# Kernel tuning notes

Hardware: AMD Instinct MI355X
Metric: run time of the kernel (lower is better)

Reference implementation:

```python
import jax, jax.numpy as jnp
import numpy as np

NUM_C, BS, L, D, M = 4096, 32, 512, 128, 50
TA, TB, TC = 0.075, 0.088, 1.0  # triangular membership params


def setup_inputs() -> dict:
    key = jax.random.key(0)
    ks = jax.random.split(key, 16)
    g = lambda i, shape, s: jax.random.normal(ks[i], shape, jnp.float32) * s
    return {
        "q": jax.random.randint(ks[0], (BS, L), 0, NUM_C),
        "r": jax.random.randint(ks[1], (BS, L), 0, 2),
        "k_emb": g(2, (NUM_C, D), 1.0),
        "Mk": g(3, (M, D), (2.0 / D) ** 0.5),
        "Mv0": g(4, (M, D), (2.0 / D) ** 0.5),
        "f_W": g(5, (D, 2 * D), (1.0 / (2 * D)) ** 0.5),
        "f_b": jnp.zeros((D,), jnp.float32),
        "a_W": g(6, (D, NUM_C + D), (1.0 / (NUM_C + D)) ** 0.5),
        "a_b": jnp.zeros((D,), jnp.float32),
        "e_W": g(7, (D, D), (2.0 / D) ** 0.5),
        "e_b": jnp.zeros((D,), jnp.float32),
        "add_W": g(8, (D, D), (2.0 / D) ** 0.5),
        "add_b": jnp.zeros((D,), jnp.float32),
        "Wih": g(9, (4 * D, D), (1.0 / D) ** 0.5),
        "Whh": g(10, (4 * D, D), (1.0 / D) ** 0.5),
        "bih": jnp.zeros((4 * D,), jnp.float32),
        "bhh": jnp.zeros((4 * D,), jnp.float32),
        "p_W": g(11, (1, D), (1.0 / D) ** 0.5),
        "p_b": jnp.zeros((1,), jnp.float32),
    }


def _forward(q, r, k_emb, Mk, Mv0, f_W, f_b, a_W, a_b, e_W, e_b,
             add_W, add_b, Wih, Whh, bih, bhh, p_W, p_b):
    B, T = q.shape
    k = k_emb[q]                                    # (B,L,D) key embeddings
    # a_embed = Linear(num_c + dim_s, dim_s) on concat(one_hot(q)*r, f):
    # split the weight so the one-hot matmul becomes a gather.
    a_Wq, a_Wf = a_W[:, :NUM_C], a_W[:, NUM_C:]
    yq = a_Wq.T[q] * r[..., None].astype(k.dtype)   # (B,L,D)

    def mem_step(Mv, xs):
        k_t, yq_t = xs                              # (B,D), (B,D)
        w = jax.nn.softmax(k_t @ Mk.T, axis=1)      # (B,M) addressing
        read = jnp.einsum('bm,bmd->bd', w, Mv)      # weighted read
        f = jnp.tanh(jnp.concatenate([read, k_t], 1) @ f_W.T + f_b)
        y = yq_t + f @ a_Wf.T + a_b                 # write content
        e = jax.nn.sigmoid(y @ e_W.T + e_b)         # erase gate
        a = jnp.tanh(y @ add_W.T + add_b)           # add vector
        Mv = Mv * (1.0 - w[:, :, None] * e[:, None, :]) + w[:, :, None] * a[:, None, :]
        return Mv, (w, f)

    Mv0b = jnp.broadcast_to(Mv0, (B, M, D))
    _, (w_all, f_all) = jax.lax.scan(
        mem_step, Mv0b, (k.transpose(1, 0, 2), yq.transpose(1, 0, 2)))
    w_all = w_all.transpose(1, 0, 2)                # (B,L,M)
    f_all = f_all.transpose(1, 0, 2)                # (B,L,D)

    # triangular membership -> ternary identity vectors {0,1,2}
    tw = jnp.maximum(jnp.minimum((w_all - TA) / (TB - TA),
                                 (TC - w_all) / (TC - TB)), 0.0)
    iv = jnp.where(tw >= 0.6, 2.0, jnp.where(tw >= 0.1, 1.0, 0.0))
    sq = jnp.sum(iv * iv, axis=2)                   # (B,L)
    dist = sq[:, :, None] + sq[:, None, :] - 2.0 * jnp.einsum('bim,bjm->bij', iv, iv)
    NEG = jnp.float32(-1e32)
    dist = jnp.where(dist > 0.0, NEG, dist)
    ut = jnp.triu(jnp.ones((T, T), bool), k=0)      # mask j >= i
    dist = jnp.where(ut[None], NEG, dist)
    idx = jnp.arange(T * T, dtype=dist.dtype).reshape(T, T)
    final = dist + idx[None]                        # (B,L,L)
    matched = jnp.max(final, axis=2) >= 0.0         # (B,L) has identical prev step
    prev = jnp.argmax(final, axis=2)                # (B,L) most recent identical t'

    # hop-LSTM: reuse hidden/cell state of previous identical timestep
    barange = jnp.arange(B)
    h0 = jnp.zeros((B, D), k.dtype)
    H0 = jnp.zeros((T, B, D), k.dtype)

    def lstm_step(carry, xs):
        h, c, H, C = carry
        t, f_t, m_t, p_t = xs
        h_in = jnp.where(m_t[:, None], H[p_t, barange], h)
        c_in = jnp.where(m_t[:, None], C[p_t, barange], c)
        gates = f_t @ Wih.T + bih + h_in @ Whh.T + bhh
        i_g, f_g, g_g, o_g = jnp.split(gates, 4, axis=1)  # torch order i,f,g,o
        c_new = jax.nn.sigmoid(f_g) * c_in + jax.nn.sigmoid(i_g) * jnp.tanh(g_g)
        h_new = jax.nn.sigmoid(o_g) * jnp.tanh(c_new)
        return (h_new, c_new, H.at[t].set(h_new), C.at[t].set(c_new)), h_new

    _, h_all = jax.lax.scan(
        lstm_step, (h0, h0, H0, H0),
        (jnp.arange(T), f_all.transpose(1, 0, 2), matched.T, prev.T))
    h_all = h_all.transpose(1, 0, 2)                # (B,L,D)
    # dropout is identity in eval mode
    p = jax.nn.sigmoid(h_all @ p_W.T + p_b)[..., 0]  # (B,L)
    return p


def reference(q, r, k_emb, Mk, Mv0, f_W, f_b, a_W, a_b, e_W, e_b,
              add_W, add_b, Wih, Whh, bih, bhh, p_W, p_b):
    return _forward(q, r, k_emb, Mk, Mv0, f_W, f_b, a_W, a_b, e_W, e_b,
                    add_W, add_b, Wih, Whh, bih, bhh, p_W, p_b)
```

## Files before the change

### kernel.cpp

```cpp
#include <hip/hip_runtime.h>
#include <cstdint>
#include <cstddef>

#define NUM_C 4096
#define BB 32
#define TT 512
#define DD 128
#define MM 50

using ull = unsigned long long;

__device__ __forceinline__ float sigmoidf_(float x){ return 1.0f/(1.0f + expf(-x)); }

__device__ __forceinline__ float fexp2_(float x){ return __builtin_amdgcn_exp2f(x); }
__device__ __forceinline__ float frcp_(float x){ return __builtin_amdgcn_rcpf(x); }
__device__ __forceinline__ float fast_sig_(float x){
  return frcp_(1.0f + fexp2_(-1.44269504088896341f*x));
}
__device__ __forceinline__ float fast_tanh_(float x){
  float t = fexp2_(2.88539008177792681f*x);
  return 1.0f - 2.0f*frcp_(t + 1.0f);
}

__device__ __forceinline__ float quadSum_(float v){
  int t = __builtin_amdgcn_update_dpp(0, __float_as_int(v), 0xB1, 0xF, 0xF, true);
  v += __int_as_float(t);
  t = __builtin_amdgcn_update_dpp(0, __float_as_int(v), 0x4E, 0xF, 0xF, true);
  v += __int_as_float(t);
  return v;
}

__device__ __forceinline__ void barL_(){
  asm volatile("s_waitcnt lgkmcnt(0)\n\ts_barrier" ::: "memory");
}
__device__ __forceinline__ void waitVM_(){
  asm volatile("s_waitcnt vmcnt(0)" ::: "memory");
}

__global__ __launch_bounds__(256) void kPre(
    const int* __restrict__ q, const int* __restrict__ r,
    const float* __restrict__ k_emb, const float* __restrict__ Mk,
    const float* __restrict__ f_W, const float* __restrict__ f_b,
    const float* __restrict__ a_W, const float* __restrict__ a_b,
    float* __restrict__ wAll, ull* __restrict__ keyLo, ull* __restrict__ keyHi,
    float* __restrict__ fpre, float* __restrict__ ypre)
{
  const int b = blockIdx.y, t0 = blockIdx.x * 32, tid = threadIdx.x;
  __shared__ __align__(16) float sK[32*129];
  __shared__ int sQ[32];
  __shared__ int sR[32];
  __shared__ union UU {
    struct { float sMk[MM*129]; double sZ[32*MM]; } p2;
    float sW2[128*65];
  } u;

  if (tid < 32){ sQ[tid] = q[b*TT + t0 + tid]; sR[tid] = r[b*TT + t0 + tid]; }
  __syncthreads();
  for (int i = tid; i < 32*128; i += 256){
    int tl = i >> 7, j = i & 127;
    sK[tl*129 + j] = k_emb[(size_t)sQ[tl]*DD + j];
  }
  for (int i = tid; i < MM*128; i += 256){
    int m = i >> 7, j = i & 127;
    u.p2.sMk[m*129 + j] = Mk[i];
  }
  __syncthreads();

  for (int idx = tid; idx < 32*MM; idx += 256){
    int tl = idx / MM, m = idx - tl*MM;
    double z = 0.0;
    for (int j = 0; j < DD; j++)
      z += (double)sK[tl*129 + j] * (double)u.p2.sMk[m*129 + j];
    u.p2.sZ[tl*MM + m] = z;
  }
  __syncthreads();

  {
    int tl = tid >> 3, l8 = tid & 7;
    double zmax = -1e300;
    for (int m = l8; m < MM; m += 8) zmax = fmax(zmax, u.p2.sZ[tl*MM + m]);
    for (int s = 1; s < 8; s <<= 1) zmax = fmax(zmax, __shfl_xor(zmax, s));
    double se = 0.0;
    for (int m = l8; m < MM; m += 8){
      double e = exp(u.p2.sZ[tl*MM + m] - zmax);
      u.p2.sZ[tl*MM + m] = e;
      se += e;
    }
    for (int s = 1; s < 8; s <<= 1) se += __shfl_xor(se, s);
    double inv = 1.0 / se;
    ull klo = 0, khi = 0;
    for (int m = l8; m < MM; m += 8){
      double w = u.p2.sZ[tl*MM + m] * inv;
      wAll[((size_t)(b*TT + t0 + tl))*MM + m] = (float)w;
      double tw = fmin((w - 0.075)/(0.088 - 0.075), (1.0 - w)/(1.0 - 0.088));
      tw = fmax(tw, 0.0);
      ull iv = (tw >= 0.6) ? 2ull : ((tw >= 0.1) ? 1ull : 0ull);
      if (m < 32) klo |= iv << (2*m); else khi |= iv << (2*(m-32));
    }
    for (int s = 1; s < 8; s <<= 1){ klo |= __shfl_xor(klo, s); khi |= __shfl_xor(khi, s); }
    if (l8 == 0){ keyLo[b*TT + t0 + tl] = klo; keyHi[b*TT + t0 + tl] = khi; }
  }

  {
    const int dq = tid & 31, tq = tid >> 5;
    float acc[4][4];
    #pragma unroll
    for (int a = 0; a < 4; a++){ acc[a][0]=0.f; acc[a][1]=0.f; acc[a][2]=0.f; acc[a][3]=0.f; }
    for (int jh = 0; jh < 2; jh++){
      __syncthreads();
      for (int i = tid; i < 128*64; i += 256){
        int dd = i >> 6, jj = i & 63;
        u.sW2[dd*65 + jj] = f_W[dd*256 + 128 + jh*64 + jj];
      }
      __syncthreads();
      for (int jj = 0; jj < 64; jj++){
        float kv[4], wv[4];
        #pragma unroll
        for (int a = 0; a < 4; a++) kv[a] = sK[(tq*4 + a)*129 + jh*64 + jj];
        #pragma unroll
        for (int c = 0; c < 4; c++) wv[c] = u.sW2[(dq*4 + c)*65 + jj];
        #pragma unroll
        for (int a = 0; a < 4; a++){
          acc[a][0] += kv[a]*wv[0]; acc[a][1] += kv[a]*wv[1];
          acc[a][2] += kv[a]*wv[2]; acc[a][3] += kv[a]*wv[3];
        }
      }
    }
    #pragma unroll
    for (int a = 0; a < 4; a++){
      int tl = tq*4 + a;
      #pragma unroll
      for (int c = 0; c < 4; c++){
        int d = dq*4 + c;
        fpre[((size_t)(b*TT + t0 + tl))*DD + d] = acc[a][c] + f_b[d];
      }
    }
  }

  for (int i = tid; i < 32*DD; i += 256){
    int tl = i >> 7, d = i & 127;
    ypre[((size_t)(b*TT + t0 + tl))*DD + d] =
        a_W[(size_t)d*(NUM_C + DD) + sQ[tl]] * (float)sR[tl] + a_b[d];
  }
}

__global__ __launch_bounds__(512) void kMatch(
    const ull* __restrict__ keyLo, const ull* __restrict__ keyHi, int* __restrict__ prevA)
{
  const int b = blockIdx.x, i = threadIdx.x;
  __shared__ ull slo[TT];
  __shared__ ull shi[TT];
  slo[i] = keyLo[b*TT + i];
  shi[i] = keyHi[b*TT + i];
  __syncthreads();
  const ull mylo = slo[i], myhi = shi[i];
  int found = -1;
  for (int j = i - 1; j >= 0; j--){
    if (slo[j] == mylo && shi[j] == myhi){ found = j; break; }
  }
  prevA[b*TT + i] = found;
}

__global__ __launch_bounds__(128) void kWW(
    const float* __restrict__ e_W, const float* __restrict__ add_W,
    const float* __restrict__ a_W,
    float* __restrict__ Ge, float* __restrict__ Ga)
{
  const int d = blockIdx.x;
  const int k = threadIdx.x;
  __shared__ float se[128];
  __shared__ float sa[128];
  se[k] = e_W[(size_t)d*DD + k];
  sa[k] = add_W[(size_t)d*DD + k];
  __syncthreads();
  float ge = 0.f, ga = 0.f;
  for (int j = 0; j < DD; j++){
    float af = a_W[(size_t)j*(NUM_C + DD) + NUM_C + k];
    ge += se[j]*af;
    ga += sa[j]*af;
  }
  Ge[(size_t)d*DD + k] = ge;
  Ga[(size_t)d*DD + k] = ga;
}

__global__ __launch_bounds__(256) void kEA(
    const float* __restrict__ ypre, const float* __restrict__ e_W,
    const float* __restrict__ add_W, const float* __restrict__ e_b,
    const float* __restrict__ add_b, float* __restrict__ eapre)
{
  const int jt = blockIdx.x;
  const int rt = blockIdx.y;
  const int tid = threadIdx.x;
  __shared__ float sW[64*129];
  __shared__ float sF[32*129];
  for (int i = tid; i < 64*128; i += 256){
    int jj = i >> 7, k = i & 127;
    int j = jt*64 + jj;
    sW[jj*129 + k] = (j < 128) ? e_W[(size_t)j*DD + k] : add_W[(size_t)(j-128)*DD + k];
  }
  for (int i = tid; i < 32*128; i += 256){
    int rr = i >> 7, k = i & 127;
    sF[rr*129 + k] = ypre[(size_t)(rt*32 + rr)*DD + k];
  }
  __syncthreads();
  const int jq = tid & 31, rq = tid >> 5;
  float acc[4][2];
  #pragma unroll
  for (int a = 0; a < 4; a++){ acc[a][0] = 0.f; acc[a][1] = 0.f; }
  for (int k = 0; k < 128; k++){
    float fv[4], wv[2];
    #pragma unroll
    for (int a = 0; a < 4; a++) fv[a] = sF[(rq*4 + a)*129 + k];
    wv[0] = sW[(jq*2 + 0)*129 + k];
    wv[1] = sW[(jq*2 + 1)*129 + k];
    #pragma unroll
    for (int a = 0; a < 4; a++){ acc[a][0] += fv[a]*wv[0]; acc[a][1] += fv[a]*wv[1]; }
  }
  #pragma unroll
  for (int a = 0; a < 4; a++){
    int rowi = rt*32 + rq*4 + a;
    #pragma unroll
    for (int c = 0; c < 2; c++){
      int j = jt*64 + jq*2 + c;
      float bj = (j < 128) ? e_b[j] : add_b[j - 128];
      eapre[(size_t)rowi*256 + j] = acc[a][c] + bj;
    }
  }
}

__global__ __launch_bounds__(256) void kWih4(
    const float* __restrict__ Wih, float* __restrict__ Wih4)
{
  int idx = blockIdx.x*256 + threadIdx.x;
  int j = idx >> 7, k = idx & 127;
  Wih4[(size_t)(k >> 2)*2048 + j*4 + (k & 3)] = Wih[idx];
}

__global__ __launch_bounds__(512, 2) __attribute__((amdgpu_waves_per_eu(2, 2)))
void kFused(
    const float* __restrict__ wAll, const float* __restrict__ fpre,
    const float* __restrict__ eapre, const float* __restrict__ f_W,
    const float* __restrict__ Ge, const float* __restrict__ Ga,
    const float* __restrict__ Mv0, float* __restrict__ fAll,
    const float* __restrict__ Wih4, const float* __restrict__ bih,
    const float* __restrict__ bhh, const int* __restrict__ prevA,
    const float* __restrict__ Whh, float* __restrict__ Hh,
    float* __restrict__ Ch, float* __restrict__ gpre, int* __restrict__ prog)
{
  const int tid = threadIdx.x;
  const int b = blockIdx.x & 31;
  const size_t base = (size_t)b*TT;

  __shared__ __align__(16) union SU {
    struct {
      float bufR[144]; float bufF[144]; float sW9[9*52];
      float sF8[8*128]; float sEA8[8*256]; float fO8[8*128];
    } m;
    struct { float sFc[8*128]; } g;
    struct {
      float xh[2][144]; float gbuf[8*512]; int spv[TT];
      float hRing[8*128]; float cRing[8*128];
    } l;
  } su;

  if (blockIdx.x < 32){
    const int dd = tid >> 2, kc = tid & 3, m0 = kc*13;
    const int wslot = (dd >> 5)*36 + (dd & 31);

    float mv[13];
    #pragma unroll
    for (int i = 0; i < 13; i++){
      int m = m0 + i;
      mv[i] = (m < MM) ? Mv0[(size_t)m*DD + dd] : 0.f;
    }
    float wf[32], ge[32], ga[32];
    {
      const float4* p;
      p = reinterpret_cast<const float4*>(&f_W[dd*256 + kc*32]);
      #pragma unroll
      for (int i = 0; i < 8; i++){ float4 v = p[i]; wf[4*i]=v.x; wf[4*i+1]=v.y; wf[4*i+2]=v.z; wf[4*i+3]=v.w; }
      p = reinterpret_cast<const float4*>(&Ge[(size_t)dd*DD + kc*32]);
      #pragma unroll
      for (int i = 0; i < 8; i++){ float4 v = p[i]; ge[4*i]=v.x; ge[4*i+1]=v.y; ge[4*i+2]=v.z; ge[4*i+3]=v.w; }
      p = reinterpret_cast<const float4*>(&Ga[(size_t)dd*DD + kc*32]);
      #pragma unroll
      for (int i = 0; i < 8; i++){ float4 v = p[i]; ga[4*i]=v.x; ga[4*i+1]=v.y; ga[4*i+2]=v.z; ga[4*i+3]=v.w; }
    }

    const int rr0 = tid / 50, mm0 = tid - rr0*50;
    if (tid < 18){ int rr = tid >> 1; su.m.sW9[rr*52 + 50 + (tid & 1)] = 0.f; }

    float4 pF = {0.f,0.f,0.f,0.f}, pEA = {0.f,0.f,0.f,0.f};
    float pW = 0.f;
    if (tid < 256) pF = reinterpret_cast<const float4*>(&fpre[base*DD])[tid];
    pEA = reinterpret_cast<const float4*>(&eapre[base*256])[tid];
    if (tid < 450) pW = wAll[(base + rr0)*MM + mm0];

    float wreg[13];

    for (int ch = 0; ch < TT/8; ch++){
      const int t0 = ch*8;
      if (ch){
        if (tid < 256){
          float4 v = reinterpret_cast<const float4*>(su.m.fO8)[tid];
          float* dst = &fAll[(base + t0 - 8)*DD + tid*4];
          __hip_atomic_store(dst+0, v.x, __ATOMIC_RELAXED, __HIP_MEMORY_SCOPE_AGENT);
          __hip_atomic_store(dst+1, v.y, __ATOMIC_RELAXED, __HIP_MEMORY_SCOPE_AGENT);
          __hip_atomic_store(dst+2, v.z, __ATOMIC_RELAXED, __HIP_MEMORY_SCOPE_AGENT);
          __hip_atomic_store(dst+3, v.w, __ATOMIC_RELAXED, __HIP_MEMORY_SCOPE_AGENT);
        }
      }
      if (tid < 256) reinterpret_cast<float4*>(su.m.sF8)[tid] = pF;
      reinterpret_cast<float4*>(su.m.sEA8)[tid] = pEA;
      if (tid < 450) su.m.sW9[rr0*52 + mm0] = pW;
      if (ch && tid < 256) waitVM_();
      if (t0 + 8 < TT){
        if (tid < 256) pF = reinterpret_cast<const float4*>(&fpre[(base + t0 + 8)*DD])[tid];
        pEA = reinterpret_cast<const float4*>(&eapre[(base + t0 + 8)*256])[tid];
        if (tid < 450) pW = (t0 + 8 + rr0 < TT) ? wAll[(base + t0 + 8 + rr0)*MM + mm0] : 0.f;
      }
      barL_();
      if (ch && tid == 0)
        __hip_atomic_store(&prog[b], ch, __ATOMIC_RELAXED, __HIP_MEMORY_SCOPE_AGENT);

      if (ch == 0){
        #pragma unroll
        for (int i = 0; i < 13; i++) wreg[i] = su.m.sW9[m0 + i];
        float r = 0.f;
        #pragma unroll
        for (int i = 0; i < 13; i++) r += wreg[i]*mv[i];
        r = quadSum_(r);
        if (kc == 0) su.m.bufR[wslot] = r;
        barL_();
      }

      #pragma unroll
      for (int tc = 0; tc < 8; tc++){
        float wn[13];
        #pragma unroll
        for (int i = 0; i < 13; i++) wn[i] = su.m.sW9[(tc+1)*52 + m0 + i];

        {
          const float4* x4 = reinterpret_cast<const float4*>(&su.m.bufR[kc*36]);
          float a0=0.f,a1=0.f,a2=0.f,a3=0.f;
          #pragma unroll
          for (int i = 0; i < 8; i++){
            float4 xv = x4[i];
            a0 += xv.x*wf[4*i]; a1 += xv.y*wf[4*i+1]; a2 += xv.z*wf[4*i+2]; a3 += xv.w*wf[4*i+3];
          }
          float s = quadSum_((a0+a1)+(a2+a3));
          float fval = fast_tanh_(s + su.m.sF8[tc*128 + dd]);
          if (kc == 0){
            su.m.bufF[wslot] = fval;
            su.m.fO8[tc*128 + dd] = fval;
          }
        }
        barL_();

        {
          const float4* x4 = reinterpret_cast<const float4*>(&su.m.bufF[kc*36]);
          float e0=0.f,e1=0.f,g0=0.f,g1=0.f;
          #pragma unroll
          for (int i = 0; i < 8; i++){
            float4 xv = x4[i];
            e0 += xv.x*ge[4*i];   e1 += xv.y*ge[4*i+1];
            e0 += xv.z*ge[4*i+2]; e1 += xv.w*ge[4*i+3];
            g0 += xv.x*ga[4*i];   g1 += xv.y*ga[4*i+1];
            g0 += xv.z*ga[4*i+2]; g1 += xv.w*ga[4*i+3];
          }
          float ep = quadSum_(e0 + e1);
          float ap = quadSum_(g0 + g1);
          float e_d = fast_sig_(ep + su.m.sEA8[tc*256 + dd]);
          float a_d = fast_tanh_(ap + su.m.sEA8[tc*256 + 128 + dd]);
          float rp0 = 0.f, rp1 = 0.f;
          #pragma unroll
          for (int i = 0; i < 13; i++){
            float t = __builtin_fmaf(-e_d, mv[i], a_d);
            mv[i] = __builtin_fmaf(wreg[i], t, mv[i]);
            if (i & 1) rp1 = __builtin_fmaf(wn[i], mv[i], rp1);
            else       rp0 = __builtin_fmaf(wn[i], mv[i], rp0);
          }
          float rd = quadSum_(rp0 + rp1);
          if (kc == 0) su.m.bufR[wslot] = rd;
        }
        #pragma unroll
        for (int i = 0; i < 13; i++) wreg[i] = wn[i];
        barL_();
      }
    }

    if (tid < 256){
      float4 v = reinterpret_cast<const float4*>(su.m.fO8)[tid];
      float* dst = &fAll[(base + TT - 8)*DD + tid*4];
      __hip_atomic_store(dst+0, v.x, __ATOMIC_RELAXED, __HIP_MEMORY_SCOPE_AGENT);
      __hip_atomic_store(dst+1, v.y, __ATOMIC_RELAXED, __HIP_MEMORY_SCOPE_AGENT);
      __hip_atomic_store(dst+2, v.z, __ATOMIC_RELAXED, __HIP_MEMORY_SCOPE_AGENT);
      __hip_atomic_store(dst+3, v.w, __ATOMIC_RELAXED, __HIP_MEMORY_SCOPE_AGENT);
      waitVM_();
    }
    __syncthreads();
    if (tid == 0)
      __hip_atomic_store(&prog[b], TT/8, __ATOMIC_RELAXED, __HIP_MEMORY_SCOPE_AGENT);

  } else if (blockIdx.x < 64){
    const float biasj = bih[tid] + bhh[tid];

    for (int ch = 0; ch < TT/8; ch++){
      const int t0 = ch*8;
      if (ch) __syncthreads();

      if (tid == 0){
        while (__hip_atomic_load(&prog[b], __ATOMIC_ACQUIRE, __HIP_MEMORY_SCOPE_AGENT) < ch + 1)
          __builtin_amdgcn_s_sleep(2);
      }
      __syncthreads();
      if (tid < 256){
        const float* src = &fAll[(base + t0)*DD + tid*4];
        float x0 = __hip_atomic_load(src+0, __ATOMIC_RELAXED, __HIP_MEMORY_SCOPE_AGENT);
        float x1 = __hip_atomic_load(src+1, __ATOMIC_RELAXED, __HIP_MEMORY_SCOPE_AGENT);
        float x2 = __hip_atomic_load(src+2, __ATOMIC_RELAXED, __HIP_MEMORY_SCOPE_AGENT);
        float x3 = __hip_atomic_load(src+3, __ATOMIC_RELAXED, __HIP_MEMORY_SCOPE_AGENT);
        su.g.sFc[tid*4+0] = x0; su.g.sFc[tid*4+1] = x1;
        su.g.sFc[tid*4+2] = x2; su.g.sFc[tid*4+3] = x3;
      }
      barL_();

      float acc[8];
      #pragma unroll
      for (int u = 0; u < 8; u++) acc[u] = 0.f;
      for (int k4 = 0; k4 < 32; k4++){
        float4 wv = reinterpret_cast<const float4*>(Wih4)[k4*512 + tid];
        #pragma unroll
        for (int u = 0; u < 8; u++){
          float4 fv = *reinterpret_cast<const float4*>(&su.g.sFc[u*128 + k4*4]);
          acc[u] += fv.x*wv.x; acc[u] += fv.y*wv.y;
          acc[u] += fv.z*wv.z; acc[u] += fv.w*wv.w;
        }
      }
      #pragma unroll
      for (int u = 0; u < 8; u++){
        float* dst = &gpre[(base + t0 + u)*512 + tid];
        __hip_atomic_store(dst, acc[u] + biasj, __ATOMIC_RELAXED, __HIP_MEMORY_SCOPE_AGENT);
      }
      waitVM_();
      __syncthreads();
      if (tid == 0)
        __hip_atomic_store(&prog[32 + b], ch + 1, __ATOMIC_RELAXED, __HIP_MEMORY_SCOPE_AGENT);
    }

  } else {
    const int jo = tid >> 2, kc = tid & 3;
    const int wslot = (jo >> 5)*36 + (jo & 31);

    float whh[4][32];
    #pragma unroll
    for (int g = 0; g < 4; g++){
      const float4* W4 = reinterpret_cast<const float4*>(&Whh[(size_t)(g*128 + jo)*128 + kc*32]);
      #pragma unroll
      for (int i = 0; i < 8; i++){
        float4 v = W4[i];
        whh[g][4*i] = v.x; whh[g][4*i+1] = v.y; whh[g][4*i+2] = v.z; whh[g][4*i+3] = v.w;
      }
    }

    su.l.spv[tid] = prevA[base + tid];
    if (tid < DD) su.l.xh[0][(tid >> 5)*36 + (tid & 31)] = 0.f;

    float cin_cur = 0.f;

    for (int ch = 0; ch < TT/8; ch++){
      const int t0 = ch*8;
      if (ch) __syncthreads();

      if (tid == 0){
        while (__hip_atomic_load(&prog[32 + b], __ATOMIC_ACQUIRE, __HIP_MEMORY_SCOPE_AGENT) < ch + 1)
          __builtin_amdgcn_s_sleep(2);
      }
      __syncthreads();
      {
        const float* src = &gpre[(base + t0)*512 + tid*8];
        float x0 = __hip_atomic_load(src+0, __ATOMIC_RELAXED, __HIP_MEMORY_SCOPE_AGENT);
        float x1 = __hip_atomic_load(src+1, __ATOMIC_RELAXED, __HIP_MEMORY_SCOPE_AGENT);
        float x2 = __hip_atomic_load(src+2, __ATOMIC_RELAXED, __HIP_MEMORY_SCOPE_AGENT);
        float x3 = __hip_atomic_load(src+3, __ATOMIC_RELAXED, __HIP_MEMORY_SCOPE_AGENT);
        float x4 = __hip_atomic_load(src+4, __ATOMIC_RELAXED, __HIP_MEMORY_SCOPE_AGENT);
        float x5 = __hip_atomic_load(src+5, __ATOMIC_RELAXED, __HIP_MEMORY_SCOPE_AGENT);
        float x6 = __hip_atomic_load(src+6, __ATOMIC_RELAXED, __HIP_MEMORY_SCOPE_AGENT);
        float x7 = __hip_atomic_load(src+7, __ATOMIC_RELAXED, __HIP_MEMORY_SCOPE_AGENT);
        float* d = &su.l.gbuf[tid*8];
        d[0]=x0; d[1]=x1; d[2]=x2; d[3]=x3; d[4]=x4; d[5]=x5; d[6]=x6; d[7]=x7;
      }
      barL_();

      #pragma unroll
      for (int tc = 0; tc < 8; tc++){
        const int t = t0 + tc, p = t & 1;
        if (tc) barL_();

        int pv2 = -1; float preH = 0.f, preC = 0.f;
        if (t + 1 < TT){
          pv2 = su.l.spv[t + 1];
          if (pv2 >= 0 && pv2 < t){
            if (pv2 >= t0){
              preH = su.l.hRing[(pv2 & 7)*128 + jo];
              preC = su.l.cRing[(pv2 & 7)*128 + jo];
            } else {
              preH = Hh[(base + pv2)*DD + jo];
              preC = Ch[(base + pv2)*DD + jo];
            }
          }
        }

        float gp0 = su.l.gbuf[tc*512 + jo];
        float gp1 = su.l.gbuf[tc*512 + 128 + jo];
        float gp2 = su.l.gbuf[tc*512 + 256 + jo];
        float gp3 = su.l.gbuf[tc*512 + 384 + jo];

        float a0=0.f,a1=0.f,a2=0.f,a3=0.f;
        {
          const float4* x4 = reinterpret_cast<const float4*>(&su.l.xh[p][kc*36]);
          #pragma unroll
          for (int i = 0; i < 8; i++){
            float4 xv = x4[i];
            a0 += xv.x*whh[0][4*i]; a0 += xv.y*whh[0][4*i+1]; a0 += xv.z*whh[0][4*i+2]; a0 += xv.w*whh[0][4*i+3];
            a1 += xv.x*whh[1][4*i]; a1 += xv.y*whh[1][4*i+1]; a1 += xv.z*whh[1][4*i+2]; a1 += xv.w*whh[1][4*i+3];
            a2 += xv.x*whh[2][4*i]; a2 += xv.y*whh[2][4*i+1]; a2 += xv.z*whh[2][4*i+2]; a2 += xv.w*whh[2][4*i+3];
            a3 += xv.x*whh[3][4*i]; a3 += xv.y*whh[3][4*i+1]; a3 += xv.z*whh[3][4*i+2]; a3 += xv.w*whh[3][4*i+3];
          }
        }
        a0 = quadSum_(a0); a1 = quadSum_(a1); a2 = quadSum_(a2); a3 = quadSum_(a3);

        const float ig = gp0 + a0, fg = gp1 + a1, gg = gp2 + a2, og = gp3 + a3;
        const float cn = fast_sig_(fg)*cin_cur + fast_sig_(ig)*fast_tanh_(gg);
        const float hn = fast_sig_(og)*fast_tanh_(cn);

        if (kc == 0){
          Hh[(base + t)*DD + jo] = hn;
          Ch[(base + t)*DD + jo] = cn;
          su.l.hRing[(t & 7)*128 + jo] = hn;
          su.l.cRing[(t & 7)*128 + jo] = cn;
        }

        float hin_n, cin_n;
        if (pv2 < 0 || pv2 >= t){ hin_n = hn; cin_n = cn; }
        else                     { hin_n = preH; cin_n = preC; }
        if (kc == 0) su.l.xh[1 - p][wslot] = hin_n;
        cin_cur = cin_n;
      }
    }
  }
}

__global__ __launch_bounds__(256) void kOut(
    const float* __restrict__ Hh, const float* __restrict__ p_W,
    const float* __restrict__ p_b, float* __restrict__ out)
{
  const int row = blockIdx.x*16 + (threadIdx.x >> 4);
  const int l = threadIdx.x & 15;
  const float4* h4 = reinterpret_cast<const float4*>(&Hh[(size_t)row*DD + l*8]);
  const float4* w4 = reinterpret_cast<const float4*>(&p_W[l*8]);
  float4 ha = h4[0], hb = h4[1], wa = w4[0], wb = w4[1];
  float s = ha.x*wa.x + ha.y*wa.y + ha.z*wa.z + ha.w*wa.w
          + hb.x*wb.x + hb.y*wb.y + hb.z*wb.z + hb.w*wb.w;
  s += __shfl_xor(s, 1); s += __shfl_xor(s, 2);
  s += __shfl_xor(s, 4); s += __shfl_xor(s, 8);
  if (l == 0) out[row] = sigmoidf_(s + p_b[0]);
}

extern "C" void kernel_launch(void* const* d_in, const int* in_sizes, int n_in,
                              void* d_out, int out_size, void* d_ws, size_t ws_size,
                              hipStream_t stream) {
  const int*   q     = (const int*)  d_in[0];
  const int*   r     = (const int*)  d_in[1];
  const float* k_emb = (const float*)d_in[2];
  const float* Mk    = (const float*)d_in[3];
  const float* Mv0   = (const float*)d_in[4];
  const float* f_W   = (const float*)d_in[5];
  const float* f_b   = (const float*)d_in[6];
  const float* a_W   = (const float*)d_in[7];
  const float* a_b   = (const float*)d_in[8];
  const float* e_W   = (const float*)d_in[9];
  const float* e_b   = (const float*)d_in[10];
  const float* add_W = (const float*)d_in[11];
  const float* add_b = (const float*)d_in[12];
  const float* Wih   = (const float*)d_in[13];
  const float* Whh   = (const float*)d_in[14];
  const float* bih   = (const float*)d_in[15];
  const float* bhh   = (const float*)d_in[16];
  const float* p_W   = (const float*)d_in[17];
  const float* p_b   = (const float*)d_in[18];
  float* out = (float*)d_out;

  char* ws = (char*)d_ws;
  size_t off = 0;
  auto alloc = [&](size_t bytes) -> char* {
    char* p = ws + off;
    off += (bytes + 255) & ~(size_t)255;
    return p;
  };
  float* wAll  = (float*)alloc((size_t)BB*TT*MM*4);
  float* fpre  = (float*)alloc((size_t)BB*TT*DD*4);
  float* ypre  = (float*)alloc((size_t)BB*TT*DD*4);
  float* fAll  = (float*)alloc((size_t)BB*TT*DD*4);
  float* eapre = (float*)alloc((size_t)BB*TT*256*4);
  float* gpre  = (float*)alloc((size_t)BB*TT*512*4);
  float* Hh    = (float*)alloc((size_t)BB*TT*DD*4);
  float* Ch    = (float*)alloc((size_t)BB*TT*DD*4);
  ull*   keyLo = (ull*)  alloc((size_t)BB*TT*8);
  ull*   keyHi = (ull*)  alloc((size_t)BB*TT*8);
  int*   prevA = (int*)  alloc((size_t)BB*TT*4);
  float* Ge    = (float*)alloc((size_t)DD*DD*4);
  float* Ga    = (float*)alloc((size_t)DD*DD*4);
  float* Wih4  = (float*)alloc((size_t)512*DD*4);
  int*   prog  = (int*)  alloc(512);
  (void)ws_size; (void)in_sizes; (void)n_in; (void)out_size;

  hipMemsetAsync(prog, 0, 64*sizeof(int), stream);
  kPre  <<<dim3(16, 32), 256, 0, stream>>>(q, r, k_emb, Mk, f_W, f_b, a_W, a_b,
                                           wAll, keyLo, keyHi, fpre, ypre);
  kWW   <<<128, 128, 0, stream>>>(e_W, add_W, a_W, Ge, Ga);
  kEA   <<<dim3(4, 512), 256, 0, stream>>>(ypre, e_W, add_W, e_b, add_b, eapre);
  kWih4 <<<256, 256, 0, stream>>>(Wih, Wih4);
  kMatch<<<32, 512, 0, stream>>>(keyLo, keyHi, prevA);
  kFused<<<96, 512, 0, stream>>>(wAll, fpre, eapre, f_W, Ge, Ga, Mv0, fAll,
                                 Wih4, bih, bhh, prevA, Whh, Hh, Ch, gpre, prog);
  kOut  <<<(BB*TT)/16, 256, 0, stream>>>(Hh, p_W, p_b, out);
}
```

Measured before the change: 784.7 us.

## Fold match, weight-prep and output kernels into fewer launches

```diff
diff --git a/kernel.cpp b/kernel.cpp
--- a/kernel.cpp
+++ b/kernel.cpp
@@ -144,43 +144,38 @@
   }
 }
 
-__global__ __launch_bounds__(512) void kMatch(
-    const ull* __restrict__ keyLo, const ull* __restrict__ keyHi, int* __restrict__ prevA)
-{
-  const int b = blockIdx.x, i = threadIdx.x;
-  __shared__ ull slo[TT];
-  __shared__ ull shi[TT];
-  slo[i] = keyLo[b*TT + i];
-  shi[i] = keyHi[b*TT + i];
-  __syncthreads();
-  const ull mylo = slo[i], myhi = shi[i];
-  int found = -1;
-  for (int j = i - 1; j >= 0; j--){
-    if (slo[j] == mylo && shi[j] == myhi){ found = j; break; }
-  }
-  prevA[b*TT + i] = found;
-}
-
-__global__ __launch_bounds__(128) void kWW(
+__global__ __launch_bounds__(256) void kInit(
     const float* __restrict__ e_W, const float* __restrict__ add_W,
     const float* __restrict__ a_W,
-    float* __restrict__ Ge, float* __restrict__ Ga)
+    float* __restrict__ Ge, float* __restrict__ Ga,
+    const float* __restrict__ Wih, float* __restrict__ Wih4)
 {
-  const int d = blockIdx.x;
-  const int k = threadIdx.x;
-  __shared__ float se[128];
-  __shared__ float sa[128];
-  se[k] = e_W[(size_t)d*DD + k];
-  sa[k] = add_W[(size_t)d*DD + k];
-  __syncthreads();
-  float ge = 0.f, ga = 0.f;
-  for (int j = 0; j < DD; j++){
-    float af = a_W[(size_t)j*(NUM_C + DD) + NUM_C + k];
-    ge += se[j]*af;
-    ga += sa[j]*af;
-  }
-  Ge[(size_t)d*DD + k] = ge;
-  Ga[(size_t)d*DD + k] = ga;
+  const int bx = blockIdx.x, tid = threadIdx.x;
+  if (bx < 128){
+    __shared__ float se[128];
+    __shared__ float sa[128];
+    const int d = bx;
+    if (tid < 128){
+      se[tid] = e_W[(size_t)d*DD + tid];
+      sa[tid] = add_W[(size_t)d*DD + tid];
+    }
+    __syncthreads();
+    if (tid < 128){
+      const int k = tid;
+      float ge = 0.f, ga = 0.f;
+      for (int j = 0; j < DD; j++){
+        float af = a_W[(size_t)j*(NUM_C + DD) + NUM_C + k];
+        ge += se[j]*af;
+        ga += sa[j]*af;
+      }
+      Ge[(size_t)d*DD + k] = ge;
+      Ga[(size_t)d*DD + k] = ga;
+    }
+  } else {
+    int idx = (bx - 128)*256 + tid;
+    int j = idx >> 7, k = idx & 127;
+    Wih4[(size_t)(k >> 2)*2048 + j*4 + (k & 3)] = Wih[idx];
+  }
 }
 
 __global__ __launch_bounds__(256) void kEA(
@@ -228,14 +223,6 @@
   }
 }
 
-__global__ __launch_bounds__(256) void kWih4(
-    const float* __restrict__ Wih, float* __restrict__ Wih4)
-{
-  int idx = blockIdx.x*256 + threadIdx.x;
-  int j = idx >> 7, k = idx & 127;
-  Wih4[(size_t)(k >> 2)*2048 + j*4 + (k & 3)] = Wih[idx];
-}
-
 __global__ __launch_bounds__(512, 2) __attribute__((amdgpu_waves_per_eu(2, 2)))
 void kFused(
     const float* __restrict__ wAll, const float* __restrict__ fpre,
@@ -243,9 +230,12 @@
     const float* __restrict__ Ge, const float* __restrict__ Ga,
     const float* __restrict__ Mv0, float* __restrict__ fAll,
     const float* __restrict__ Wih4, const float* __restrict__ bih,
-    const float* __restrict__ bhh, const int* __restrict__ prevA,
+    const float* __restrict__ bhh, const ull* __restrict__ keyLo,
+    const ull* __restrict__ keyHi, int* __restrict__ prevA,
     const float* __restrict__ Whh, float* __restrict__ Hh,
-    float* __restrict__ Ch, float* __restrict__ gpre, int* __restrict__ prog)
+    float* __restrict__ Ch, float* __restrict__ gpre,
+    const float* __restrict__ p_W, const float* __restrict__ p_b,
+    float* __restrict__ out, int* __restrict__ prog)
 {
   const int tid = threadIdx.x;
   const int b = blockIdx.x & 31;
@@ -256,10 +246,10 @@
       float bufR[144]; float bufF[144]; float sW9[9*52];
       float sF8[8*128]; float sEA8[8*256]; float fO8[8*128];
     } m;
-    struct { float sFc[8*128]; } g;
+    struct { float sFc[8*128]; ull slo[TT]; ull shi[TT]; } g;
     struct {
       float xh[2][144]; float gbuf[8*512]; int spv[TT];
-      float hRing[8*128]; float cRing[8*128];
+      float hRing[8*128]; float cRing[8*128]; float pw[DD];
     } l;
   } su;
 
@@ -405,10 +395,21 @@
   } else if (blockIdx.x < 64){
     const float biasj = bih[tid] + bhh[tid];
 
+    {
+      su.g.slo[tid] = keyLo[base + tid];
+      su.g.shi[tid] = keyHi[base + tid];
+      barL_();
+      const ull mylo = su.g.slo[tid], myhi = su.g.shi[tid];
+      int found = -1;
+      for (int j = tid - 1; j >= 0; j--){
+        if (su.g.slo[j] == mylo && su.g.shi[j] == myhi){ found = j; break; }
+      }
+      __hip_atomic_store(&prevA[base + tid], found, __ATOMIC_RELAXED, __HIP_MEMORY_SCOPE_AGENT);
+      waitVM_();
+    }
+
     for (int ch = 0; ch < TT/8; ch++){
       const int t0 = ch*8;
-      if (ch) __syncthreads();
-
       if (tid == 0){
         while (__hip_atomic_load(&prog[b], __ATOMIC_ACQUIRE, __HIP_MEMORY_SCOPE_AGENT) < ch + 1)
           __builtin_amdgcn_s_sleep(2);
@@ -463,20 +464,19 @@
       }
     }
 
-    su.l.spv[tid] = prevA[base + tid];
-    if (tid < DD) su.l.xh[0][(tid >> 5)*36 + (tid & 31)] = 0.f;
-
     float cin_cur = 0.f;
 
     for (int ch = 0; ch < TT/8; ch++){
       const int t0 = ch*8;
-      if (ch) __syncthreads();
-
       if (tid == 0){
         while (__hip_atomic_load(&prog[32 + b], __ATOMIC_ACQUIRE, __HIP_MEMORY_SCOPE_AGENT) < ch + 1)
           __builtin_amdgcn_s_sleep(2);
       }
       __syncthreads();
+      if (ch == 0){
+        su.l.spv[tid] = __hip_atomic_load(&prevA[base + tid], __ATOMIC_RELAXED, __HIP_MEMORY_SCOPE_AGENT);
+        if (tid < DD) su.l.xh[0][(tid >> 5)*36 + (tid & 31)] = 0.f;
+      }
       {
         const float* src = &gpre[(base + t0)*512 + tid*8];
         float x0 = __hip_atomic_load(src+0, __ATOMIC_RELAXED, __HIP_MEMORY_SCOPE_AGENT);
@@ -548,23 +548,23 @@
         cin_cur = cin_n;
       }
     }
-  }
-}
-
-__global__ __launch_bounds__(256) void kOut(
-    const float* __restrict__ Hh, const float* __restrict__ p_W,
-    const float* __restrict__ p_b, float* __restrict__ out)
-{
-  const int row = blockIdx.x*16 + (threadIdx.x >> 4);
-  const int l = threadIdx.x & 15;
-  const float4* h4 = reinterpret_cast<const float4*>(&Hh[(size_t)row*DD + l*8]);
-  const float4* w4 = reinterpret_cast<const float4*>(&p_W[l*8]);
-  float4 ha = h4[0], hb = h4[1], wa = w4[0], wb = w4[1];
-  float s = ha.x*wa.x + ha.y*wa.y + ha.z*wa.z + ha.w*wa.w
-          + hb.x*wb.x + hb.y*wb.y + hb.z*wb.z + hb.w*wb.w;
-  s += __shfl_xor(s, 1); s += __shfl_xor(s, 2);
-  s += __shfl_xor(s, 4); s += __shfl_xor(s, 8);
-  if (l == 0) out[row] = sigmoidf_(s + p_b[0]);
+
+    __syncthreads();
+    if (tid < DD) su.l.pw[tid] = p_W[tid];
+    barL_();
+    {
+      const int t = tid;
+      const float* hrow = &Hh[(base + t)*DD];
+      float s = 0.f;
+      #pragma unroll
+      for (int k4 = 0; k4 < 32; k4++){
+        float4 hv = *reinterpret_cast<const float4*>(&hrow[k4*4]);
+        const float* wp = &su.l.pw[k4*4];
+        s += hv.x*wp[0] + hv.y*wp[1] + hv.z*wp[2] + hv.w*wp[3];
+      }
+      out[base + t] = sigmoidf_(s + p_b[0]);
+    }
+  }
 }
 
 extern "C" void kernel_launch(void* const* d_in, const int* in_sizes, int n_in,
@@ -618,11 +618,9 @@
   hipMemsetAsync(prog, 0, 64*sizeof(int), stream);
   kPre  <<<dim3(16, 32), 256, 0, stream>>>(q, r, k_emb, Mk, f_W, f_b, a_W, a_b,
                                            wAll, keyLo, keyHi, fpre, ypre);
-  kWW   <<<128, 128, 0, stream>>>(e_W, add_W, a_W, Ge, Ga);
+  kInit <<<384, 256, 0, stream>>>(e_W, add_W, a_W, Ge, Ga, Wih, Wih4);
   kEA   <<<dim3(4, 512), 256, 0, stream>>>(ypre, e_W, add_W, e_b, add_b, eapre);
-  kWih4 <<<256, 256, 0, stream>>>(Wih, Wih4);
-  kMatch<<<32, 512, 0, stream>>>(keyLo, keyHi, prevA);
   kFused<<<96, 512, 0, stream>>>(wAll, fpre, eapre, f_W, Ge, Ga, Mv0, fAll,
-                                 Wih4, bih, bhh, prevA, Whh, Hh, Ch, gpre, prog);
-  kOut  <<<(BB*TT)/16, 256, 0, stream>>>(Hh, p_W, p_b, out);
-}
+                                 Wih4, bih, bhh, keyLo, keyHi, prevA, Whh,
+                                 Hh, Ch, gpre, p_W, p_b, out, prog);
+}
```

Result: faster. 758.5 us (-3.3%).
